# Performance work log

Measured on AMD Instinct MI355X. Metric: run time of the kernel, lower is better.

The kernel has to match this reference:

```python
import jax, jax.numpy as jnp
import numpy as np

NUM_TASKS = 150
ACT_DIM = 4
ENC_DIM = 256
EMB_DIM = 32
HEAD_HID = 128
B, H, W = 256, 128, 128


def _conv(x, w, b):
    # x: NCHW, w: OIHW, stride 2, padding 1 (torch Conv2d semantics)
    y = jax.lax.conv_general_dilated(x, w, window_strides=(2, 2),
                                     padding=((1, 1), (1, 1)),
                                     dimension_numbers=('NCHW', 'OIHW', 'NCHW'))
    return y + b[None, :, None, None]


def setup_inputs() -> dict:
    key = jax.random.key(0)
    ks = iter(jax.random.split(key, 32))
    s = 0.05
    d = {
        'images': jax.random.normal(next(ks), (B, 3, H, W), jnp.float32),
        'proprioception': jax.random.normal(next(ks), (B, 7), jnp.float32),
        'task_ids': jax.random.randint(next(ks), (B,), 0, NUM_TASKS, jnp.int32),
        # vision encoder convs (OIHW)
        'c1_w': jax.random.normal(next(ks), (64, 3, 3, 3), jnp.float32) * s,
        'c1_b': jnp.zeros((64,), jnp.float32),
        'c2_w': jax.random.normal(next(ks), (128, 64, 3, 3), jnp.float32) * s,
        'c2_b': jnp.zeros((128,), jnp.float32),
        'c3_w': jax.random.normal(next(ks), (256, 128, 3, 3), jnp.float32) * s,
        'c3_b': jnp.zeros((256,), jnp.float32),
        # proprioception encoder (weights stored as [in, out])
        'p1_w': jax.random.normal(next(ks), (7, 64), jnp.float32) * s,
        'p1_b': jnp.zeros((64,), jnp.float32),
        'p2_w': jax.random.normal(next(ks), (64, 64), jnp.float32) * s,
        'p2_b': jnp.zeros((64,), jnp.float32),
        # shared-encoder fusion MLP (320 -> 256 -> 256)
        'f1_w': jax.random.normal(next(ks), (256 + 64, ENC_DIM), jnp.float32) * s,
        'f1_b': jnp.zeros((ENC_DIM,), jnp.float32),
        'f2_w': jax.random.normal(next(ks), (ENC_DIM, ENC_DIM), jnp.float32) * s,
        'f2_b': jnp.zeros((ENC_DIM,), jnp.float32),
        # task embedding table
        'task_emb': jax.random.normal(next(ks), (NUM_TASKS, EMB_DIM), jnp.float32) * s,
        # policy-level fusion (288 -> 256), dropout is identity at inference
        'g_w': jax.random.normal(next(ks), (ENC_DIM + EMB_DIM, ENC_DIM), jnp.float32) * s,
        'g_b': jnp.zeros((ENC_DIM,), jnp.float32),
        # stacked task-specific heads [num_tasks, in, out]
        'h1_w': jax.random.normal(next(ks), (NUM_TASKS, ENC_DIM, HEAD_HID), jnp.float32) * s,
        'h1_b': jnp.zeros((NUM_TASKS, HEAD_HID), jnp.float32),
        'h2_w': jax.random.normal(next(ks), (NUM_TASKS, HEAD_HID, HEAD_HID), jnp.float32) * s,
        'h2_b': jnp.zeros((NUM_TASKS, HEAD_HID), jnp.float32),
        'h3_w': jax.random.normal(next(ks), (NUM_TASKS, HEAD_HID, ACT_DIM), jnp.float32) * s,
        'h3_b': jnp.zeros((NUM_TASKS, ACT_DIM), jnp.float32),
    }
    return d


def reference(images, proprioception, task_ids,
              c1_w, c1_b, c2_w, c2_b, c3_w, c3_b,
              p1_w, p1_b, p2_w, p2_b,
              f1_w, f1_b, f2_w, f2_b,
              task_emb, g_w, g_b,
              h1_w, h1_b, h2_w, h2_b, h3_w, h3_b):
    relu = jax.nn.relu
    # vision encoder: 3 strided convs + global avg pool (AdaptiveAvgPool2d(1,1))
    v = relu(_conv(images, c1_w, c1_b))
    v = relu(_conv(v, c2_w, c2_b))
    v = relu(_conv(v, c3_w, c3_b))
    v = jnp.mean(v, axis=(2, 3))                      # [B, 256]
    # proprioception encoder (no final ReLU)
    p = relu(proprioception @ p1_w + p1_b) @ p2_w + p2_b  # [B, 64]
    # shared fusion
    f = relu(jnp.concatenate([v, p], axis=1) @ f1_w + f1_b)
    f = relu(f @ f2_w + f2_b)                         # [B, 256]
    # task embedding + policy fusion (dropout = identity in eval)
    e = task_emb[task_ids]                            # [B, 32]
    z = relu(jnp.concatenate([f, e], axis=1) @ g_w + g_b)  # [B, 256]
    # routed task heads: gather per-sample expert params, batched matmuls
    a = relu(jnp.einsum('bd,bdh->bh', z, h1_w[task_ids]) + h1_b[task_ids])
    a = relu(jnp.einsum('bd,bdh->bh', a, h2_w[task_ids]) + h2_b[task_ids])
    a = jnp.einsum('bd,bdh->bh', a, h3_w[task_ids]) + h3_b[task_ids]  # [B, 4]
    return a
```

## Files before the change

kernel.cpp:

```cpp
#include <hip/hip_runtime.h>
#include <hip/hip_bf16.h>

#define DIV_UP(a,b) (((a)+(b)-1)/(b))

typedef __attribute__((ext_vector_type(8))) short short8;
typedef __attribute__((ext_vector_type(4))) float f32x4;

__device__ __forceinline__ ushort bf16_bits(float x) {
    return __builtin_bit_cast(ushort, __float2bfloat16(x));
}

__global__ __launch_bounds__(256) void halo_zero_kernel(
    uint4* __restrict__ act1, uint4* __restrict__ act2,
    float4* __restrict__ vbuf) {
    const int b = blockIdx.x, tid = threadIdx.x;
    const uint4 z = {0u, 0u, 0u, 0u};
    uint4* a1 = act1 + (size_t)b * 33800;
    for (int i = tid; i < 520; i += 256) a1[i] = z;
    for (int i = tid; i < 512; i += 256) {
        int r = (i >> 3) + 1;
        a1[r * 520 + (i & 7)] = z;
    }
    uint4* a2 = act2 + (size_t)b * 17424;
    for (int i = tid; i < 528; i += 256) a2[i] = z;
    for (int i = tid; i < 512; i += 256) {
        int r = (i >> 4) + 1;
        a2[r * 528 + (i & 15)] = z;
    }
    int idx = b * 256 + tid;
    float4 zf = {0.f, 0.f, 0.f, 0.f};
    if (idx < 16384) vbuf[idx] = zf;
}

__global__ void repack_w1_kernel(const float* __restrict__ src,
                                 __hip_bfloat16* __restrict__ dst) {
    int t = blockIdx.x * blockDim.x + threadIdx.x;
    if (t >= 2048) return;
    int k  = t & 31;
    int oc = t >> 5;
    dst[t] = (k < 27) ? __float2bfloat16(src[oc * 27 + k])
                      : __float2bfloat16(0.f);
}

__global__ void repack_w_kernel(const float* __restrict__ src,
                                __hip_bfloat16* __restrict__ dst, int O, int C) {
    int t = blockIdx.x * blockDim.x + threadIdx.x;
    if (t >= O * C * 9) return;
    int e   = t & 7;
    int r   = t >> 3;
    int n   = r % O;
    int q   = r / O;
    int SEG = C >> 3;
    int sg  = q % SEG;
    int tap = q / SEG;
    dst[t] = __float2bfloat16(src[(n * C + sg * 8 + e) * 9 + tap]);
}

__global__ __launch_bounds__(256) void conv1_mfma_kernel(
    const float* __restrict__ in,
    const __hip_bfloat16* __restrict__ wB,
    const float* __restrict__ bias,
    __hip_bfloat16* __restrict__ out) {
    const int tid  = threadIdx.x;
    const int lane = tid & 63;
    const int wv   = tid >> 6;
    const int l15  = lane & 15;
    const int quad = lane >> 4;
    const int tile = blockIdx.x;
    const int b    = blockIdx.y;
    const int oh0  = tile << 2;

    __shared__ __align__(16) char smem[36864];
    float*  sx = (float*)smem;
    ushort* Al = (ushort*)(smem + 14256);
    ushort* Cs = (ushort*)smem;

    const float* ip  = in + (size_t)b * 3 * 128 * 128;
    const int    ih0 = 2 * oh0 - 1;
    for (int e = tid; e < 3510; e += 256) {
        int c   = e / 1170;
        int rem = e - c * 1170;
        int r   = rem / 130;
        int col = rem - r * 130;
        int ih  = ih0 + r;
        int iw  = col - 1;
        bool ok = ((unsigned)ih < 128u) && ((unsigned)iw < 128u);
        sx[(c * 9 + r) * 132 + col] = ok ? ip[c * 16384 + ih * 128 + iw] : 0.f;
    }
    __syncthreads();

    {
        const int px = tid, ohl = px >> 6, ow = px & 63;
        union { uint4 u4[4]; ushort us[32]; } rowv;
#pragma unroll
        for (int k = 0; k < 27; ++k) {
            const int c = k / 9, rm = k - c * 9, kh = rm / 3, kw = rm - kh * 3;
            rowv.us[k] = bf16_bits(sx[(c * 9 + 2 * ohl + kh) * 132 + 2 * ow + kw]);
        }
#pragma unroll
        for (int k = 27; k < 32; ++k) rowv.us[k] = 0;
#pragma unroll
        for (int q = 0; q < 4; ++q)
            *(uint4*)(Al + px * 32 + (((q ^ (px >> 1)) & 3) << 3)) = rowv.u4[q];
    }
    __syncthreads();

    short8 af[4], bf[4];
#pragma unroll
    for (int i = 0; i < 4; ++i)
        af[i] = __builtin_bit_cast(short8,
            *(const uint4*)(wB + ((i * 16 + l15) * 32 + quad * 8)));
#pragma unroll
    for (int j = 0; j < 4; ++j) {
        int p = wv * 64 + j * 16 + l15;
        bf[j] = __builtin_bit_cast(short8,
            *(const uint4*)(Al + p * 32 + (((quad ^ (p >> 1)) & 3) << 3)));
    }
    f32x4 acc[4][4];
#pragma unroll
    for (int i = 0; i < 4; ++i)
#pragma unroll
        for (int j = 0; j < 4; ++j)
            acc[i][j] = __builtin_amdgcn_mfma_f32_16x16x32_bf16(
                af[i], bf[j], (f32x4){0.f, 0.f, 0.f, 0.f}, 0, 0, 0);

    float4 bv[4];
#pragma unroll
    for (int i = 0; i < 4; ++i)
        bv[i] = *(const float4*)(bias + i * 16 + quad * 4);

    __syncthreads();

#pragma unroll
    for (int j = 0; j < 4; ++j) {
        const int px = wv * 64 + j * 16 + l15;
#pragma unroll
        for (int i = 0; i < 4; ++i) {
            union { uint2 u2; ushort us[4]; } pk;
#pragma unroll
            for (int r = 0; r < 4; ++r)
                pk.us[r] = bf16_bits(
                    fmaxf(acc[i][j][r] + ((const float*)&bv[i])[r], 0.f));
            *(uint2*)(Cs + px * 72 + i * 16 + quad * 4) = pk.u2;
        }
    }
    __syncthreads();

    __hip_bfloat16* ob = out + (((size_t)b * 65 + oh0 + 1) * 65 + 1) * 64;
#pragma unroll
    for (int it = 0; it < 8; ++it) {
        int g   = it * 256 + tid;
        int px  = g >> 3, cq = g & 7;
        uint4 v = *(const uint4*)(Cs + px * 72 + cq * 8);
        int ohl = px >> 6, ow = px & 63;
        *(uint4*)(ob + ((size_t)ohl * 65 + ow) * 64 + cq * 8) = v;
    }
}

__global__ __launch_bounds__(256, 2) void conv2_gemm_kernel(
    const __hip_bfloat16* __restrict__ act,
    const __hip_bfloat16* __restrict__ wtB,
    const float* __restrict__ bias,
    __hip_bfloat16* __restrict__ out) {
    const int tid  = threadIdx.x;
    const int lane = tid & 63;
    const int w    = tid >> 6;
    const int l15  = lane & 15;
    const int quad = lane >> 4;
    const int per  = gridDim.x >> 3;
    const int Mt   = (blockIdx.x & 7) * per + (blockIdx.x >> 3);
    const int bimg = Mt >> 3;
    const int oh0  = (Mt & 7) << 2;

    __shared__ __align__(16) char smem[37504];
    ushort* As = (ushort*)smem;
    ushort* Cs = (ushort*)smem;

    f32x4 acc[4][4];
#pragma unroll
    for (int i = 0; i < 4; ++i)
#pragma unroll
        for (int j = 0; j < 4; ++j) acc[i][j] = (f32x4){0.f, 0.f, 0.f, 0.f};

    const int wm = (w & 1) << 6;
    const int wn = (w >> 1) << 6;
    const size_t abase = ((size_t)(bimg * 65 + 2 * oh0)) * 65 * 64;

    for (int h = 0; h < 2; ++h) {
        __syncthreads();
#pragma unroll
        for (int it = 0; it < 10; ++it) {
            int e = tid + (it << 8);
            if (e < 2340) {
                int s = e & 3, p = e >> 2;
                uint4 val = *(const uint4*)(act + abase + (size_t)p * 64 +
                                            h * 32 + s * 8);
                *(uint4*)(As + p * 32 + (((s ^ (p >> 1)) & 3) << 3)) = val;
            }
        }
        __syncthreads();
#pragma unroll
        for (int tap = 0; tap < 9; ++tap) {
            const int kh = tap / 3, kw = tap - kh * 3;
            short8 af[4], bf[4];
#pragma unroll
            for (int i = 0; i < 4; ++i) {
                int ml = wm + i * 16 + l15;
                int p  = ((ml >> 5) * 2 + kh) * 65 + ((ml & 31) * 2 + kw);
                af[i] = __builtin_bit_cast(short8,
                    *(const uint4*)(As + p * 32 + (((quad ^ (p >> 1)) & 3) << 3)));
            }
#pragma unroll
            for (int j = 0; j < 4; ++j)
                bf[j] = __builtin_bit_cast(short8,
                    *(const uint4*)(wtB +
                        ((size_t)((tap * 8 + h * 4 + quad) * 128) +
                         wn + j * 16 + l15) * 8));
#pragma unroll
            for (int i = 0; i < 4; ++i)
#pragma unroll
                for (int j = 0; j < 4; ++j)
                    acc[i][j] = __builtin_amdgcn_mfma_f32_16x16x32_bf16(
                        af[i], bf[j], acc[i][j], 0, 0, 0);
        }
    }

    __syncthreads();
#pragma unroll
    for (int j = 0; j < 4; ++j) {
        int n = wn + j * 16 + l15;
        float bv = bias[n];
#pragma unroll
        for (int i = 0; i < 4; ++i)
#pragma unroll
            for (int r = 0; r < 4; ++r) {
                int ml = wm + i * 16 + quad * 4 + r;
                Cs[ml * 132 + n] = bf16_bits(fmaxf(acc[i][j][r] + bv, 0.f));
            }
    }
    __syncthreads();
#pragma unroll
    for (int q = 0; q < 16; ++q) {
        int c   = tid + 256 * q;
        int row = c >> 5;
        int off = c & 31;
        uint2 val = *(const uint2*)(Cs + row * 132 + off * 4);
        int m  = (Mt << 7) + row;
        int b  = m >> 10;
        int rr = m & 1023;
        int oh = rr >> 5;
        int ow = rr & 31;
        size_t pix = ((size_t)(b * 33 + oh + 1) * 33 + (ow + 1));
        *(uint2*)(out + pix * 128 + off * 4) = val;
    }
}

__global__ __launch_bounds__(256, 2) void conv3_gemm_pool_kernel(
    const __hip_bfloat16* __restrict__ act,
    const __hip_bfloat16* __restrict__ wtB,
    const float* __restrict__ bias,
    float* __restrict__ v ) {
    const int tid  = threadIdx.x;
    const int lane = tid & 63;
    const int w    = tid >> 6;
    const int l15  = lane & 15;
    const int quad = lane >> 4;
    const int per  = gridDim.x >> 3;
    const int Mt   = (blockIdx.x & 7) * per + (blockIdx.x >> 3);
    const int bimg = Mt >> 2;
    const int oh0  = (Mt & 3) << 2;

    __shared__ __align__(16) char smem[38016];
    ushort* As   = (ushort*)smem;
    float*  sred = (float*)smem;

    f32x4 acc[4][4];
#pragma unroll
    for (int i = 0; i < 4; ++i)
#pragma unroll
        for (int j = 0; j < 4; ++j) acc[i][j] = (f32x4){0.f, 0.f, 0.f, 0.f};

    const int wn = w << 6;
    const size_t abase = ((size_t)(bimg * 33 + 2 * oh0)) * 33 * 128;

    for (int h = 0; h < 2; ++h) {
        __syncthreads();
#pragma unroll
        for (int it = 0; it < 10; ++it) {
            int e = tid + (it << 8);
            if (e < 2376) {
                int s = e & 7, p = e >> 3;
                uint4 val = *(const uint4*)(act + abase + (size_t)p * 128 +
                                            h * 64 + s * 8);
                *(uint4*)(As + p * 64 + (((s ^ (p >> 1)) & 7) << 3)) = val;
            }
        }
        __syncthreads();
#pragma unroll 1
        for (int tap = 0; tap < 9; ++tap) {
            const int kh = tap / 3, kw = tap - kh * 3;
#pragma unroll
            for (int ks = 0; ks < 2; ++ks) {
                short8 af[4], bf[4];
                const int sl = ks * 4 + quad;
#pragma unroll
                for (int i = 0; i < 4; ++i) {
                    int p = (i * 2 + kh) * 33 + l15 * 2 + kw;
                    af[i] = __builtin_bit_cast(short8,
                        *(const uint4*)(As + p * 64 +
                                        (((sl ^ (p >> 1)) & 7) << 3)));
                }
#pragma unroll
                for (int j = 0; j < 4; ++j)
                    bf[j] = __builtin_bit_cast(short8,
                        *(const uint4*)(wtB +
                            ((size_t)((tap * 16 + h * 8 + sl) * 256) +
                             wn + j * 16 + l15) * 8));
#pragma unroll
                for (int i = 0; i < 4; ++i)
#pragma unroll
                    for (int j = 0; j < 4; ++j)
                        acc[i][j] = __builtin_amdgcn_mfma_f32_16x16x32_bf16(
                            af[i], bf[j], acc[i][j], 0, 0, 0);
            }
        }
    }

    float s4[4];
#pragma unroll
    for (int j = 0; j < 4; ++j) {
        float bv = bias[wn + j * 16 + l15];
        float s = 0.f;
#pragma unroll
        for (int i = 0; i < 4; ++i)
#pragma unroll
            for (int r = 0; r < 4; ++r)
                s += fmaxf(acc[i][j][r] + bv, 0.f);
        s += __shfl_xor(s, 16, 64);
        s += __shfl_xor(s, 32, 64);
        s4[j] = s;
    }
    __syncthreads();
    if (quad == 0) {
#pragma unroll
        for (int j = 0; j < 4; ++j) sred[wn + j * 16 + l15] = s4[j];
    }
    __syncthreads();
    atomicAdd(v + (size_t)bimg * 256 + tid, sred[tid] * (1.f / 256.f));
}

template<int N, int K, int S, bool RELU>
__device__ __forceinline__ void gemv_stage(const float* __restrict__ w,
                                           const float* __restrict__ bias,
                                           const float* in, float* outv,
                                           float4* red4, int tid) {
    constexpr int G = N / 4;
    constexpr int CHK = K / S;
    static_assert(G * S == 256 && CHK * S == K, "stage shape");
    const int g = tid % G, s = tid / G;
    const float4* wp = (const float4*)w;
    float4 a; a.x = a.y = a.z = a.w = 0.f;
    const int k0 = s * CHK;
#pragma unroll 8
    for (int i = 0; i < CHK; ++i) {
        float x = in[k0 + i];
        float4 wv = wp[(size_t)(k0 + i) * G + g];
        a.x = fmaf(x, wv.x, a.x);
        a.y = fmaf(x, wv.y, a.y);
        a.z = fmaf(x, wv.z, a.z);
        a.w = fmaf(x, wv.w, a.w);
    }
    red4[tid] = a;
    __syncthreads();
    if (tid < N) {
        int gg = tid >> 2, e = tid & 3;
        float vv = bias[tid];
#pragma unroll
        for (int ss = 0; ss < S; ++ss) {
            const float* rp = (const float*)(red4 + ss * G + gg);
            vv += rp[e];
        }
        if (RELU) vv = fmaxf(vv, 0.f);
        outv[tid] = vv;
    }
    __syncthreads();
}

__global__ __launch_bounds__(256) void tail_kernel(
    const float* __restrict__ prop, const int* __restrict__ task_ids,
    const float* __restrict__ p1_w, const float* __restrict__ p1_b,
    const float* __restrict__ p2_w, const float* __restrict__ p2_b,
    const float* __restrict__ v,
    const float* __restrict__ f1_w, const float* __restrict__ f1_b,
    const float* __restrict__ f2_w, const float* __restrict__ f2_b,
    const float* __restrict__ task_emb,
    const float* __restrict__ g_w, const float* __restrict__ g_b,
    const float* __restrict__ h1_w, const float* __restrict__ h1_b,
    const float* __restrict__ h2_w, const float* __restrict__ h2_b,
    const float* __restrict__ h3_w, const float* __restrict__ h3_b,
    float* __restrict__ out) {
    const int b   = blockIdx.x;
    const int tid = threadIdx.x;
    const int t   = task_ids[b];
    __shared__ float sa[320];
    __shared__ float sb[288];
    __shared__ float sph[64];
    __shared__ float4 red4[256];

    sa[tid] = (tid < 256) ? v[(size_t)b * 256 + tid] : 0.f;
    if (tid < 64) {
        float h = p1_b[tid];
#pragma unroll
        for (int k = 0; k < 7; ++k) h = fmaf(prop[b * 7 + k], p1_w[k * 64 + tid], h);
        sph[tid] = fmaxf(h, 0.f);
    }
    __syncthreads();
    gemv_stage<64, 64, 16, false>(p2_w, p2_b, sph, sa + 256, red4, tid);
    gemv_stage<256, 320, 4, true>(f1_w, f1_b, sa, sb, red4, tid);
    gemv_stage<256, 256, 4, true>(f2_w, f2_b, sb, sa, red4, tid);
    if (tid < 32) sa[256 + tid] = task_emb[t * 32 + tid];
    __syncthreads();
    gemv_stage<256, 288, 4, true>(g_w, g_b, sa, sb, red4, tid);
    gemv_stage<128, 256, 8, true>(h1_w + (size_t)t * 32768, h1_b + t * 128,
                                  sb, sa, red4, tid);
    gemv_stage<128, 128, 8, true>(h2_w + (size_t)t * 16384, h2_b + t * 128,
                                  sa, sb, red4, tid);
    if (tid < 128) {
        float4 wv = ((const float4*)(h3_w + (size_t)t * 512))[tid];
        float x = sb[tid];
        float r0 = x * wv.x, r1 = x * wv.y, r2 = x * wv.z, r3 = x * wv.w;
#pragma unroll
        for (int off = 1; off < 64; off <<= 1) {
            r0 += __shfl_xor(r0, off, 64);
            r1 += __shfl_xor(r1, off, 64);
            r2 += __shfl_xor(r2, off, 64);
            r3 += __shfl_xor(r3, off, 64);
        }
        if ((tid & 63) == 0) {
            float4 rv; rv.x = r0; rv.y = r1; rv.z = r2; rv.w = r3;
            red4[tid >> 6] = rv;
        }
    }
    __syncthreads();
    if (tid < 4) {
        const float* ra = (const float*)(red4 + 0);
        const float* rb = (const float*)(red4 + 1);
        out[b * 4 + tid] = ra[tid] + rb[tid] + h3_b[t * 4 + tid];
    }
}

extern "C" void kernel_launch(void* const* d_in, const int* in_sizes, int n_in,
                              void* d_out, int out_size, void* d_ws, size_t ws_size,
                              hipStream_t stream) {
    (void)in_sizes; (void)n_in; (void)out_size;
    const float* images   = (const float*)d_in[0];
    const float* prop     = (const float*)d_in[1];
    const int*   task_ids = (const int*)d_in[2];
    const float* c1_w = (const float*)d_in[3];
    const float* c1_b = (const float*)d_in[4];
    const float* c2_w = (const float*)d_in[5];
    const float* c2_b = (const float*)d_in[6];
    const float* c3_w = (const float*)d_in[7];
    const float* c3_b = (const float*)d_in[8];
    const float* p1_w = (const float*)d_in[9];
    const float* p1_b = (const float*)d_in[10];
    const float* p2_w = (const float*)d_in[11];
    const float* p2_b = (const float*)d_in[12];
    const float* f1_w = (const float*)d_in[13];
    const float* f1_b = (const float*)d_in[14];
    const float* f2_w = (const float*)d_in[15];
    const float* f2_b = (const float*)d_in[16];
    const float* temb = (const float*)d_in[17];
    const float* g_w  = (const float*)d_in[18];
    const float* g_b  = (const float*)d_in[19];
    const float* h1_w = (const float*)d_in[20];
    const float* h1_b = (const float*)d_in[21];
    const float* h2_w = (const float*)d_in[22];
    const float* h2_b = (const float*)d_in[23];
    const float* h3_w = (const float*)d_in[24];
    const float* h3_b = (const float*)d_in[25];
    float* out = (float*)d_out;

    const size_t per_img = (size_t)65 * 65 * 64 * 2 + (size_t)33 * 33 * 128 * 2;
    const size_t fixed   = (size_t)256 * 256 * 4 + 1728 * 4 +
                           (size_t)73728 * 2 + (size_t)294912 * 2 + 4096;
    int CHI = 64;
    if (ws_size >= fixed + per_img * 256) CHI = 256;
    else if (ws_size >= fixed + per_img * 128) CHI = 128;

    char* ws = (char*)d_ws;
    size_t off = 0;
    auto alloc = [&](size_t bytes) {
        void* p = ws + off;
        off += (bytes + 255) & ~(size_t)255;
        return p;
    };
    __hip_bfloat16* act1 = (__hip_bfloat16*)alloc((size_t)CHI * 65 * 65 * 64 * 2);
    __hip_bfloat16* act2 = (__hip_bfloat16*)alloc((size_t)CHI * 33 * 33 * 128 * 2);
    float*          vbuf = (float*)alloc((size_t)256 * 256 * 4);
    __hip_bfloat16* w1b  = (__hip_bfloat16*)alloc((size_t)2048 * 2);
    __hip_bfloat16* w2t  = (__hip_bfloat16*)alloc((size_t)73728 * 2);
    __hip_bfloat16* w3t  = (__hip_bfloat16*)alloc((size_t)294912 * 2);

    halo_zero_kernel<<<dim3(CHI), 256, 0, stream>>>(
        (uint4*)act1, (uint4*)act2, (float4*)vbuf);
    repack_w1_kernel<<<8, 256, 0, stream>>>(c1_w, w1b);
    repack_w_kernel<<<DIV_UP(73728, 256), 256, 0, stream>>>(c2_w, w2t, 128, 64);
    repack_w_kernel<<<DIV_UP(294912, 256), 256, 0, stream>>>(c3_w, w3t, 256, 128);

    for (int c0 = 0; c0 < 256; c0 += CHI) {
        const float* img_c = images + (size_t)c0 * 3 * 128 * 128;
        conv1_mfma_kernel<<<dim3(16, CHI), dim3(256), 0, stream>>>(
            img_c, w1b, c1_b, act1);
        conv2_gemm_kernel<<<dim3(CHI * 8), 256, 0, stream>>>(
            act1, w2t, c2_b, act2);
        conv3_gemm_pool_kernel<<<dim3(CHI * 4), 256, 0, stream>>>(
            act2, w3t, c3_b, vbuf + (size_t)c0 * 256);
    }
    tail_kernel<<<256, 256, 0, stream>>>(prop, task_ids, p1_w, p1_b, p2_w, p2_b,
                                         vbuf, f1_w, f1_b, f2_w, f2_b, temb,
                                         g_w, g_b, h1_w, h1_b, h2_w, h2_b,
                                         h3_w, h3_b, out);
}
```

Measured before the change: 367.1 us.

## Load full conv input tiles directly into LDS with global_load_lds

In the conv2 and conv3 GEMM kernels, the two per-K-half tile loads that went through registers are replaced by a single up-front pass of `global_load_lds` 16-byte transfers. This fills both channel halves into a doubled LDS buffer. The XOR swizzle moves to the global source address, and the fragment reads are re-indexed to match. The aim is to remove register staging and one load/sync round, but LDS per block grows to about 76 KB. The fixed 19-iteration loop also reads somewhat past the needed tile, which risks out-of-bounds reads on the last tile.

```diff
diff --git a/kernel.cpp b/kernel.cpp
--- a/kernel.cpp
+++ b/kernel.cpp
@@ -8,6 +8,12 @@
 
 __device__ __forceinline__ ushort bf16_bits(float x) {
     return __builtin_bit_cast(ushort, __float2bfloat16(x));
+}
+
+__device__ __forceinline__ void gload_lds16(const ushort* g, ushort* l) {
+    __builtin_amdgcn_global_load_lds(
+        (const __attribute__((address_space(1))) void*)g,
+        (__attribute__((address_space(3))) void*)l, 16, 0, 0);
 }
 
 __global__ __launch_bounds__(256) void halo_zero_kernel(
@@ -172,7 +178,7 @@
     const int bimg = Mt >> 3;
     const int oh0  = (Mt & 7) << 2;
 
-    __shared__ __align__(16) char smem[37504];
+    __shared__ __align__(16) char smem[77824];
     ushort* As = (ushort*)smem;
     ushort* Cs = (ushort*)smem;
 
@@ -185,20 +191,21 @@
     const int wm = (w & 1) << 6;
     const int wn = (w >> 1) << 6;
     const size_t abase = ((size_t)(bimg * 65 + 2 * oh0)) * 65 * 64;
+    const ushort* ap = (const ushort*)act;
+
+#pragma unroll
+    for (int it = 0; it < 19; ++it) {
+        int c  = (it << 8) + tid;
+        int p  = c >> 3;
+        int t  = c & 7;
+        int h  = t >> 2;
+        int ss = (t & 3) ^ ((p >> 1) & 3);
+        gload_lds16(ap + abase + (size_t)p * 64 + h * 32 + ss * 8,
+                    As + (size_t)c * 8);
+    }
+    __syncthreads();
 
     for (int h = 0; h < 2; ++h) {
-        __syncthreads();
-#pragma unroll
-        for (int it = 0; it < 10; ++it) {
-            int e = tid + (it << 8);
-            if (e < 2340) {
-                int s = e & 3, p = e >> 2;
-                uint4 val = *(const uint4*)(act + abase + (size_t)p * 64 +
-                                            h * 32 + s * 8);
-                *(uint4*)(As + p * 32 + (((s ^ (p >> 1)) & 3) << 3)) = val;
-            }
-        }
-        __syncthreads();
 #pragma unroll
         for (int tap = 0; tap < 9; ++tap) {
             const int kh = tap / 3, kw = tap - kh * 3;
@@ -208,7 +215,8 @@
                 int ml = wm + i * 16 + l15;
                 int p  = ((ml >> 5) * 2 + kh) * 65 + ((ml & 31) * 2 + kw);
                 af[i] = __builtin_bit_cast(short8,
-                    *(const uint4*)(As + p * 32 + (((quad ^ (p >> 1)) & 3) << 3)));
+                    *(const uint4*)(As + p * 64 + h * 32 +
+                                    (((quad ^ (p >> 1)) & 3) << 3)));
             }
 #pragma unroll
             for (int j = 0; j < 4; ++j)
@@ -270,7 +278,7 @@
     const int bimg = Mt >> 2;
     const int oh0  = (Mt & 3) << 2;
 
-    __shared__ __align__(16) char smem[38016];
+    __shared__ __align__(16) char smem[77824];
     ushort* As   = (ushort*)smem;
     float*  sred = (float*)smem;
 
@@ -282,20 +290,21 @@
 
     const int wn = w << 6;
     const size_t abase = ((size_t)(bimg * 33 + 2 * oh0)) * 33 * 128;
+    const ushort* ap = (const ushort*)act;
+
+#pragma unroll
+    for (int it = 0; it < 19; ++it) {
+        int c  = (it << 8) + tid;
+        int p  = c >> 4;
+        int t  = c & 15;
+        int h  = t >> 3;
+        int ss = (t & 7) ^ ((p >> 1) & 7);
+        gload_lds16(ap + abase + (size_t)p * 128 + h * 64 + ss * 8,
+                    As + (size_t)c * 8);
+    }
+    __syncthreads();
 
     for (int h = 0; h < 2; ++h) {
-        __syncthreads();
-#pragma unroll
-        for (int it = 0; it < 10; ++it) {
-            int e = tid + (it << 8);
-            if (e < 2376) {
-                int s = e & 7, p = e >> 3;
-                uint4 val = *(const uint4*)(act + abase + (size_t)p * 128 +
-                                            h * 64 + s * 8);
-                *(uint4*)(As + p * 64 + (((s ^ (p >> 1)) & 7) << 3)) = val;
-            }
-        }
-        __syncthreads();
 #pragma unroll 1
         for (int tap = 0; tap < 9; ++tap) {
             const int kh = tap / 3, kw = tap - kh * 3;
@@ -307,7 +316,7 @@
                 for (int i = 0; i < 4; ++i) {
                     int p = (i * 2 + kh) * 33 + l15 * 2 + kw;
                     af[i] = __builtin_bit_cast(short8,
-                        *(const uint4*)(As + p * 64 +
+                        *(const uint4*)(As + p * 128 + h * 64 +
                                         (((sl ^ (p >> 1)) & 7) << 3)));
                 }
 #pragma unroll
```

Measured after the change: 352.8 us. -3.9%, faster.
